# Performance work log

Hardware: AMD Instinct MI355X
Metric: run time of the kernel (lower is better)

The kernel has to match this reference:

```python
import jax, jax.numpy as jnp
import numpy as np

NUM_ANCHORS_LIST = [6400, 1600, 400]  # 640x640 input, strides 8/16/32
STRIDES = [8, 16, 32]
GRID_SIZES = [80, 40, 20]
TOPK = 9
EPS = 1e-9


def _make_anchor_bboxes():
    boxes = []
    for stride, size in zip(STRIDES, GRID_SIZES):
        c = (np.arange(size, dtype=np.float32) + 0.5) * stride
        cx, cy = np.meshgrid(c, c)
        half = stride / 2.0
        b = np.stack([cx - half, cy - half, cx + half, cy + half], axis=-1)
        boxes.append(b.reshape(-1, 4))
    return jnp.asarray(np.concatenate(boxes, axis=0))  # [8400,4]


def _random_boxes(key, shape_prefix, img=640.0):
    k1, k2 = jax.random.split(key)
    cxy = jax.random.uniform(k1, shape_prefix + (2,), minval=0.0, maxval=img)
    wh = jax.random.uniform(k2, shape_prefix + (2,), minval=8.0, maxval=160.0)
    x1y1 = jnp.clip(cxy - wh / 2, 0.0, img)
    x2y2 = jnp.clip(cxy + wh / 2, 0.0, img)
    return jnp.concatenate([x1y1, x2y2], axis=-1).astype(jnp.float32)


def setup_inputs() -> dict:
    key = jax.random.key(0)
    kg, kp, kl, km = jax.random.split(key, 4)
    B, N, M, C = 16, 8400, 128, 80
    return {
        "anchor_bboxes": _make_anchor_bboxes(),               # [N,4]
        "gt_labels": jax.random.randint(kl, (B, M, 1), 0, C).astype(jnp.int64),
        "gt_bboxes": _random_boxes(kg, (B, M)),               # [B,M,4]
        "mask_gt": jax.random.randint(km, (B, M, 1), 0, 2).astype(jnp.int32),
        "pred_bboxes": _random_boxes(kp, (B, N)),             # [B,N,4]
        "num_classes": C,
    }


def _batch_bbox_iou(box1, box2):
    # box1 [B,N,4], box2 [B,M,4] -> [B,N,M]
    area1 = (box1[..., 2] - box1[..., 0]) * (box1[..., 3] - box1[..., 1])
    area2 = (box2[..., 2] - box2[..., 0]) * (box2[..., 3] - box2[..., 1])
    ix1 = jnp.maximum(box1[:, :, None, 0], box2[:, None, :, 0])
    iy1 = jnp.maximum(box1[:, :, None, 1], box2[:, None, :, 1])
    ix2 = jnp.minimum(box1[:, :, None, 2], box2[:, None, :, 2])
    iy2 = jnp.minimum(box1[:, :, None, 3], box2[:, None, :, 3])
    inter = jnp.maximum(ix2 - ix1, 0.0) * jnp.maximum(iy2 - iy1, 0.0)
    union = area1[:, :, None] + area2[:, None, :] - inter
    return inter / (union + EPS)


def reference(anchor_bboxes, gt_labels, gt_bboxes, mask_gt, pred_bboxes, num_classes):
    B, M = gt_bboxes.shape[0], gt_bboxes.shape[1]
    N = anchor_bboxes.shape[0]
    labels = gt_labels[..., 0].astype(jnp.int32)           # [B,M]

    ac = (anchor_bboxes[:, :2] + anchor_bboxes[:, 2:]) / 2  # [N,2]
    gc = (gt_bboxes[..., :2] + gt_bboxes[..., 2:]) / 2      # [B,M,2]
    # cdist via expanded quadratic form (avoids [B,N,M,2] intermediate)
    a2 = jnp.sum(ac * ac, axis=-1)                          # [N]
    g2 = jnp.sum(gc * gc, axis=-1)                          # [B,M]
    d2 = a2[None, :, None] + g2[:, None, :] - 2.0 * jnp.einsum('nc,bmc->bnm', ac, gc)
    distances = jnp.sqrt(jnp.maximum(d2, 0.0))              # [B,N,M]

    # per-level topk closest anchors per GT -> candidate mask [B,N,M]
    bidx = jnp.arange(B)[:, None, None]
    midx = jnp.arange(M)[None, :, None]
    level_masks = []
    start = 0
    for ln in NUM_ANCHORS_LIST:
        ld = distances[:, start:start + ln, :]               # [B,ln,M]
        k = min(TOPK, ln)
        _, idx = jax.lax.top_k(-jnp.swapaxes(ld, 1, 2), k)   # [B,M,k] anchor idx
        lm = jnp.zeros((B, ln, M), dtype=bool).at[bidx, idx, midx].set(True)
        level_masks.append(lm)
        start += ln
    candidate_mask = jnp.concatenate(level_masks, axis=1)    # [B,N,M]

    ious = _batch_bbox_iou(jnp.broadcast_to(anchor_bboxes[None], (B, N, 4)), gt_bboxes)
    cm_f = candidate_mask.astype(ious.dtype)
    cand_ious = ious * cm_f
    count = jnp.maximum(cm_f.sum(axis=1), 1.0)               # [B,M]
    mean = cand_ious.sum(axis=1) / count
    sq_mean = jnp.sum(cand_ious * cand_ious, axis=1) / count # mask is 0/1
    std = jnp.sqrt(jnp.maximum(sq_mean - mean * mean, 0.0))
    thr = mean + std                                         # [B,M]

    is_pos = candidate_mask & (ious >= thr[:, None, :])
    center_in_gt = ((ac[None, :, None, 0] >= gt_bboxes[:, None, :, 0])
                    & (ac[None, :, None, 0] <= gt_bboxes[:, None, :, 2])
                    & (ac[None, :, None, 1] >= gt_bboxes[:, None, :, 1])
                    & (ac[None, :, None, 1] <= gt_bboxes[:, None, :, 3]))
    is_pos = is_pos & center_in_gt & (mask_gt[..., 0] > 0)[:, None, :]

    fg_mask = jnp.any(is_pos, axis=-1)                       # [B,N]
    pos_ious = jnp.where(is_pos, ious, 0.0)
    max_gt_idx = jnp.argmax(pos_ious, axis=-1)               # [B,N]

    fg_f = fg_mask.astype(ious.dtype)
    assigned_labels = jnp.take_along_axis(labels, max_gt_idx, axis=1) * fg_mask.astype(jnp.int32)
    assigned_bboxes = jnp.take_along_axis(gt_bboxes, max_gt_idx[..., None], axis=1) * fg_f[..., None]
    assigned_ious = jnp.take_along_axis(ious, max_gt_idx[..., None], axis=2)[..., 0] * fg_f

    pred_ious = _batch_bbox_iou(pred_bboxes, gt_bboxes)
    pred_assigned = jnp.take_along_axis(pred_ious, max_gt_idx[..., None], axis=2)[..., 0] * fg_f
    assigned_ious = assigned_ious * pred_assigned

    assigned_scores = jax.nn.one_hot(assigned_labels, num_classes, dtype=ious.dtype) \
        * (assigned_ious * fg_f)[..., None]                  # [B,N,C]
    return assigned_labels, assigned_bboxes, assigned_scores, fg_mask
```

## Files before the change

kernel.cpp:

```cpp
#include <hip/hip_runtime.h>
#include <stdint.h>

#define B_ 16
#define N_ 8400
#define M_ 128

__device__ __forceinline__ float iou_box(float ax1, float ay1, float ax2, float ay2,
                                         float bx1, float by1, float bx2, float by2) {
    float area1 = __fmul_rn(__fsub_rn(ax2, ax1), __fsub_rn(ay2, ay1));
    float area2 = __fmul_rn(__fsub_rn(bx2, bx1), __fsub_rn(by2, by1));
    float ix1 = fmaxf(ax1, bx1), iy1 = fmaxf(ay1, by1);
    float ix2 = fminf(ax2, bx2), iy2 = fminf(ay2, by2);
    float iw = fmaxf(__fsub_rn(ix2, ix1), 0.0f);
    float ih = fmaxf(__fsub_rn(iy2, iy1), 0.0f);
    float inter = __fmul_rn(iw, ih);
    float uni = __fsub_rn(__fadd_rn(area1, area2), inter);
    return __fdiv_rn(inter, __fadd_rn(uni, 1e-9f));
}

__global__ __launch_bounds__(192) void assign_kernel(
    const float* __restrict__ gt_bboxes,
    const int* __restrict__ mask_gt,
    unsigned long long* __restrict__ ws) {
    const int g = blockIdx.x;
    if (mask_gt[g] == 0) return;
    const int b = g >> 7;
    const int m = g & (M_ - 1);
    const int t = threadIdx.x;
    const int w = t >> 6;
    const int lane = t & 63;

    __shared__ int   s_idx[27];
    __shared__ float s_iou[27];
    __shared__ int   s_cin[27];
    __shared__ float s_thr;

    const float4 gb = ((const float4*)gt_bboxes)[g];
    const float gx1 = gb.x, gy1 = gb.y, gx2 = gb.z, gy2 = gb.w;
    const float gcx = __fmul_rn(__fadd_rn(gx1, gx2), 0.5f);
    const float gcy = __fmul_rn(__fadd_rn(gy1, gy2), 0.5f);
    const float g2 = __fadd_rn(__fmul_rn(gcx, gcx), __fmul_rn(gcy, gcy));

    const int   size  = (w == 0) ? 80 : ((w == 1) ? 40 : 20);
    const int   start = (w == 0) ? 0 : ((w == 1) ? 6400 : 8000);
    const float st    = (w == 0) ? 8.0f : ((w == 1) ? 16.0f : 32.0f);
    const float inv   = (w == 0) ? 0.125f : ((w == 1) ? 0.0625f : 0.03125f);

    int jl = (int)floorf(gcx * inv - 0.5f) - 2;
    int il = (int)floorf(gcy * inv - 0.5f) - 2;
    jl = min(max(jl, 0), size - 6);
    il = min(max(il, 0), size - 6);

    unsigned long long key = ~0ULL;
    if (lane < 36) {
        const int wy = lane / 6;
        const int wx = lane - wy * 6;
        const int   i   = il + wy;
        const int   j   = jl + wx;
        const float acy = __fmul_rn(__fadd_rn((float)i, 0.5f), st);
        const float acx = __fmul_rn(__fadd_rn((float)j, 0.5f), st);
        const int   n   = start + i * size + j;
        float a2  = __fadd_rn(__fmul_rn(acx, acx), __fmul_rn(acy, acy));
        float dot = __fadd_rn(__fmul_rn(acx, gcx), __fmul_rn(acy, gcy));
        float d2  = __fsub_rn(__fadd_rn(a2, g2), __fmul_rn(2.0f, dot));
        float dist = __fsqrt_rn(fmaxf(d2, 0.0f));
        key = ((unsigned long long)__float_as_uint(dist) << 32) | (unsigned)n;
    }

#pragma unroll
    for (int k = 2; k <= 64; k <<= 1) {
#pragma unroll
        for (int j = k >> 1; j > 0; j >>= 1) {
            unsigned long long other = __shfl_xor(key, j, 64);
            const bool up = ((lane & k) == 0);
            const bool keepMin = (((lane & j) == 0) == up);
            const unsigned long long mn = key < other ? key : other;
            const unsigned long long mx = key < other ? other : key;
            key = keepMin ? mn : mx;
        }
    }
    if (lane < 9) s_idx[w * 9 + lane] = (int)(key & 0xFFFFFFFFu);
    __syncthreads();

    if (t < 3) {
        int v[9];
#pragma unroll
        for (int k = 0; k < 9; ++k) v[k] = s_idx[t * 9 + k];
#pragma unroll
        for (int rr = 0; rr < 9; ++rr) {
#pragma unroll
            for (int p = (rr & 1); p + 1 < 9; p += 2) {
                int lo = min(v[p], v[p + 1]);
                int hi = max(v[p], v[p + 1]);
                v[p] = lo; v[p + 1] = hi;
            }
        }
#pragma unroll
        for (int k = 0; k < 9; ++k) s_idx[t * 9 + k] = v[k];
    }
    __syncthreads();

    if (t < 27) {
        const int   l      = t / 9;
        const int   size2  = (l == 0) ? 80 : ((l == 1) ? 40 : 20);
        const int   start2 = (l == 0) ? 0 : ((l == 1) ? 6400 : 8000);
        const float st2    = (l == 0) ? 8.0f : ((l == 1) ? 16.0f : 32.0f);
        const float half   = __fmul_rn(st2, 0.5f);
        const int n = s_idx[t];
        const int loc = n - start2;
        const int i = loc / size2;
        const int j = loc - i * size2;
        float acx = __fmul_rn(__fadd_rn((float)j, 0.5f), st2);
        float acy = __fmul_rn(__fadd_rn((float)i, 0.5f), st2);
        float ax1 = __fsub_rn(acx, half), ay1 = __fsub_rn(acy, half);
        float ax2 = __fadd_rn(acx, half), ay2 = __fadd_rn(acy, half);
        float iou = iou_box(ax1, ay1, ax2, ay2, gx1, gy1, gx2, gy2);
        s_iou[t] = iou;
        s_cin[t] = (acx >= gx1 && acx <= gx2 && acy >= gy1 && acy <= gy2) ? 1 : 0;
    }
    __syncthreads();

    if (t == 0) {
        float tot = 0.0f, tot2 = 0.0f;
#pragma unroll
        for (int kk = 0; kk < 27; ++kk) {
            const float iou = s_iou[kk];
            tot  = __fadd_rn(tot, iou);
            tot2 = __fadd_rn(tot2, __fmul_rn(iou, iou));
        }
        float mean = __fdiv_rn(tot, 27.0f);
        float sqm  = __fdiv_rn(tot2, 27.0f);
        float var  = __fsub_rn(sqm, __fmul_rn(mean, mean));
        float stdv = __fsqrt_rn(fmaxf(var, 0.0f));
        s_thr = __fadd_rn(mean, stdv);
    }
    __syncthreads();

    if (t < 27) {
        const float iou = s_iou[t];
        if (s_cin[t] && iou >= s_thr) {
            unsigned long long packed =
                ((unsigned long long)(0xC0000000u | __float_as_uint(iou)) << 32) |
                (unsigned long long)(0xFFFFFFFFu - (unsigned)m);
            atomicMax(&ws[(size_t)b * N_ + s_idx[t]], packed);
        }
    }
}

__global__ __launch_bounds__(256) void finalize_kernel(
    const int* __restrict__ gt_labels,
    const float* __restrict__ gt_bboxes,
    const float* __restrict__ pred_bboxes,
    const int* __restrict__ num_classes_p,
    const unsigned long long* __restrict__ ws,
    float* __restrict__ out) {
    const int t = threadIdx.x;
    const int idx = blockIdx.x * 256 + t;
    const int b = idx / N_;
    const int C = num_classes_p[0];

    __shared__ int   s_slab[256];
    __shared__ float s_sv[256];
    __shared__ int   s_sfg[256];

    const unsigned long long w = ws[idx];
    const bool fg = (w >> 62) == 3ULL;
    float labelf = 0.0f;
    float4 bb = make_float4(0.f, 0.f, 0.f, 0.f);
    float v = 0.0f, fgf = 0.0f;
    int label = 0;
    if (fg) {
        fgf = 1.0f;
        const unsigned mm = 0xFFFFFFFFu - (unsigned)(w & 0xFFFFFFFFu);
        const float a_iou = __uint_as_float((unsigned)((w >> 32) & 0x3FFFFFFFu));
        label = gt_labels[b * M_ + (int)mm];
        labelf = (float)label;
        const float* gg = gt_bboxes + ((size_t)b * M_ + mm) * 4;
        bb.x = gg[0]; bb.y = gg[1]; bb.z = gg[2]; bb.w = gg[3];
        const float* p = pred_bboxes + (size_t)idx * 4;
        float piou = iou_box(p[0], p[1], p[2], p[3], bb.x, bb.y, bb.z, bb.w);
        v = __fmul_rn(a_iou, piou);
    }

    out[idx] = labelf;
    ((float4*)(out + (size_t)B_ * N_))[idx] = bb;
    out[(size_t)B_ * N_ * (5 + C) + idx] = fgf;

    s_slab[t] = label;
    s_sv[t]   = v;
    s_sfg[t]  = fg ? 1 : 0;
    __syncthreads();

    const int c4 = C >> 2;
    const int total4 = 256 * c4;
    float4* sc = (float4*)(out + (size_t)B_ * N_ * 5) + (size_t)blockIdx.x * 256 * c4;
    for (int f = t; f < total4; f += 256) {
        const int a = f / c4;
        const int q = f - a * c4;
        float4 z = make_float4(0.f, 0.f, 0.f, 0.f);
        if (s_sfg[a]) {
            const int c0 = q << 2;
            const int La = s_slab[a];
            if (La >= c0 && La < c0 + 4) ((float*)&z)[La - c0] = s_sv[a];
        }
        sc[f] = z;
    }
}

extern "C" void kernel_launch(void* const* d_in, const int* in_sizes, int n_in,
                              void* d_out, int out_size, void* d_ws, size_t ws_size,
                              hipStream_t stream) {
    const int*   gt_labels  = (const int*)d_in[1];
    const float* gt_bboxes  = (const float*)d_in[2];
    const int*   mask_gt    = (const int*)d_in[3];
    const float* pred       = (const float*)d_in[4];
    const int*   ncls       = (const int*)d_in[5];
    unsigned long long* ws  = (unsigned long long*)d_ws;
    float* out              = (float*)d_out;

    assign_kernel<<<B_ * M_, 192, 0, stream>>>(gt_bboxes, mask_gt, ws);
    finalize_kernel<<<(B_ * N_) / 256, 256, 0, stream>>>(
        gt_labels, gt_bboxes, pred, ncls, ws, out);
}
```

Before: 99.38 us.

## Zero score tensor inside assign kernel and scatter only foreground scores

Adds 512 extra blocks to the assign kernel that zero the whole [B,N,C] score region with float4 stores. The finalize kernel no longer writes the dense one-hot scores through shared memory; it writes one scalar per foreground anchor. The aim is to overlap the large zero-fill with the latency-bound assignment work and to remove the shared-memory pass and barrier from finalize. The extra blocks rely on hardcoded sizes (C=80) and need the zeroing to finish before finalize, which stream ordering guarantees.

```diff
diff --git a/kernel.cpp b/kernel.cpp
--- a/kernel.cpp
+++ b/kernel.cpp
@@ -4,6 +4,9 @@
 #define B_ 16
 #define N_ 8400
 #define M_ 128
+#define SC4_  2688000
+#define ZB_   512
+#define ZPER_ 5250
 
 __device__ __forceinline__ float iou_box(float ax1, float ay1, float ax2, float ay2,
                                          float bx1, float by1, float bx2, float by2) {
@@ -18,15 +21,25 @@
     return __fdiv_rn(inter, __fadd_rn(uni, 1e-9f));
 }
 
-__global__ __launch_bounds__(192) void assign_kernel(
+__global__ __launch_bounds__(256) void assign_zero_kernel(
     const float* __restrict__ gt_bboxes,
     const int* __restrict__ mask_gt,
-    unsigned long long* __restrict__ ws) {
+    unsigned long long* __restrict__ ws,
+    float* __restrict__ out) {
+    if (blockIdx.x >= 2048) {
+        float4* sp = (float4*)(out + (size_t)B_ * N_ * 5) +
+                     (size_t)(blockIdx.x - 2048) * ZPER_;
+        const float4 z4 = make_float4(0.f, 0.f, 0.f, 0.f);
+        for (int k = threadIdx.x; k < ZPER_; k += 256) sp[k] = z4;
+        return;
+    }
+
     const int g = blockIdx.x;
     if (mask_gt[g] == 0) return;
+    const int t = threadIdx.x;
+    if (t >= 192) return;
     const int b = g >> 7;
     const int m = g & (M_ - 1);
-    const int t = threadIdx.x;
     const int w = t >> 6;
     const int lane = t & 63;
 
@@ -154,14 +167,9 @@
     const int* __restrict__ num_classes_p,
     const unsigned long long* __restrict__ ws,
     float* __restrict__ out) {
-    const int t = threadIdx.x;
-    const int idx = blockIdx.x * 256 + t;
+    const int idx = blockIdx.x * 256 + threadIdx.x;
     const int b = idx / N_;
     const int C = num_classes_p[0];
-
-    __shared__ int   s_slab[256];
-    __shared__ float s_sv[256];
-    __shared__ int   s_sfg[256];
 
     const unsigned long long w = ws[idx];
     const bool fg = (w >> 62) == 3ULL;
@@ -184,27 +192,8 @@
 
     out[idx] = labelf;
     ((float4*)(out + (size_t)B_ * N_))[idx] = bb;
+    if (fg) out[(size_t)B_ * N_ * 5 + (size_t)idx * C + label] = v;
     out[(size_t)B_ * N_ * (5 + C) + idx] = fgf;
-
-    s_slab[t] = label;
-    s_sv[t]   = v;
-    s_sfg[t]  = fg ? 1 : 0;
-    __syncthreads();
-
-    const int c4 = C >> 2;
-    const int total4 = 256 * c4;
-    float4* sc = (float4*)(out + (size_t)B_ * N_ * 5) + (size_t)blockIdx.x * 256 * c4;
-    for (int f = t; f < total4; f += 256) {
-        const int a = f / c4;
-        const int q = f - a * c4;
-        float4 z = make_float4(0.f, 0.f, 0.f, 0.f);
-        if (s_sfg[a]) {
-            const int c0 = q << 2;
-            const int La = s_slab[a];
-            if (La >= c0 && La < c0 + 4) ((float*)&z)[La - c0] = s_sv[a];
-        }
-        sc[f] = z;
-    }
 }
 
 extern "C" void kernel_launch(void* const* d_in, const int* in_sizes, int n_in,
@@ -218,7 +207,7 @@
     unsigned long long* ws  = (unsigned long long*)d_ws;
     float* out              = (float*)d_out;
 
-    assign_kernel<<<B_ * M_, 192, 0, stream>>>(gt_bboxes, mask_gt, ws);
+    assign_zero_kernel<<<2048 + ZB_, 256, 0, stream>>>(gt_bboxes, mask_gt, ws, out);
     finalize_kernel<<<(B_ * N_) / 256, 256, 0, stream>>>(
         gt_labels, gt_bboxes, pred, ncls, ws, out);
 }
```

New measurement: 82.91 us. -16.6%, faster.
